# Performance work log

Hardware: AMD Instinct MI355X
Metric: run time of the kernel (lower is better)

## Reference

```python
import jax, jax.numpy as jnp
import numpy as np

NUM_HEADS = 16

def setup_inputs() -> dict:
    key = jax.random.key(0)
    ks = jax.random.split(key, 11)
    B, S, E, H, KV = 32, 4, 1024, NUM_HEADS, 4096
    d = E // H
    inp = {
        "x": jax.random.normal(ks[0], (B, S, E), dtype=jnp.float32),
        "cache_k": jax.random.normal(ks[1], (B, H, KV, d), dtype=jnp.float32),
        "cache_v": jax.random.normal(ks[2], (B, H, KV, d), dtype=jnp.float32),
        "Wq": jax.random.normal(ks[3], (E, E), dtype=jnp.float32) * (E ** -0.5),
        "bq": jax.random.normal(ks[4], (E,), dtype=jnp.float32) * 0.01,
        "Wk": jax.random.normal(ks[5], (E, E), dtype=jnp.float32) * (E ** -0.5),
        "bk": jax.random.normal(ks[6], (E,), dtype=jnp.float32) * 0.01,
        "Wv": jax.random.normal(ks[7], (E, E), dtype=jnp.float32) * (E ** -0.5),
        "bv": jax.random.normal(ks[8], (E,), dtype=jnp.float32) * 0.01,
        "Wo": jax.random.normal(ks[9], (E, E), dtype=jnp.float32) * (E ** -0.5),
        "bo": jax.random.normal(ks[10], (E,), dtype=jnp.float32) * 0.01,
    }
    return inp


def reference(x, cache_k, cache_v, Wq, bq, Wk, bk, Wv, bv, Wo, bo):
    B, S, E = x.shape
    H = NUM_HEADS
    d = E // H
    # torch Linear: y = x @ W.T + b
    def proj(W, b):
        return (x @ W.T + b).reshape(B, S, H, d).transpose(0, 2, 1, 3)  # [B,H,S,d]
    Q = proj(Wq, bq)
    K_new = proj(Wk, bk)
    V_new = proj(Wv, bv)
    K = jnp.concatenate([cache_k, K_new], axis=2)  # [B,H,KV+S,d]
    V = jnp.concatenate([cache_v, V_new], axis=2)
    scores = jnp.einsum("bhqd,bhkd->bhqk", Q, K) / jnp.sqrt(jnp.float32(d))
    attn = jax.nn.softmax(scores, axis=-1)
    out = jnp.einsum("bhqk,bhkd->bhqd", attn, V)  # [B,H,S,d]
    out = out.transpose(0, 2, 1, 3).reshape(B, S, E)
    return out @ Wo.T + bo
```

## Files before the change

### kernel.cpp

```cpp
#include <hip/hip_runtime.h>
#include <math.h>

#define B_   32
#define S_   4
#define H_   16
#define D_   64
#define E_   1024
#define KV_  4096
#define NBH  512
#define CS   512
#define NC   9
#define RECSZ 264

__global__ __launch_bounds__(256) void proj_kernel(
    const float* __restrict__ A, const float* __restrict__ W,
    const float* __restrict__ bias, float* __restrict__ out, int mode) {
    __shared__ float a_lds[4 * E_];
    __shared__ float res[256];
    const int t0 = blockIdx.x * 4;
    const int n0 = blockIdx.y * 64;
    const int tid = threadIdx.x;
    const int lane = tid & 63, wid = tid >> 6;
    const int sub = lane >> 4, cg = lane & 15, tsel = cg & 3;

    const float4* Ag = (const float4*)(A + (size_t)t0 * E_);
    float4* al = (float4*)a_lds;
    #pragma unroll
    for (int i = 0; i < 4; ++i) al[tid + 256 * i] = Ag[tid + 256 * i];
    __syncthreads();

    #pragma unroll
    for (int g = 0; g < 4; ++g) {
        const int r0 = n0 + wid * 16 + g * 4;
        const float4* wrow = (const float4*)(W + (size_t)r0 * E_);
        float ac0 = 0.f, ac1 = 0.f, ac2 = 0.f, ac3 = 0.f;
        #pragma unroll
        for (int kk = 0; kk < 16; ++kk) {
            float4 w4 = wrow[sub * 256 + kk * 16 + cg];
            float4 a0 = *(const float4*)&a_lds[0 * E_ + kk * 64 + cg * 4];
            float4 a1 = *(const float4*)&a_lds[1 * E_ + kk * 64 + cg * 4];
            float4 a2 = *(const float4*)&a_lds[2 * E_ + kk * 64 + cg * 4];
            float4 a3 = *(const float4*)&a_lds[3 * E_ + kk * 64 + cg * 4];
            ac0 += w4.x * a0.x + w4.y * a0.y + w4.z * a0.z + w4.w * a0.w;
            ac1 += w4.x * a1.x + w4.y * a1.y + w4.z * a1.z + w4.w * a1.w;
            ac2 += w4.x * a2.x + w4.y * a2.y + w4.z * a2.z + w4.w * a2.w;
            ac3 += w4.x * a3.x + w4.y * a3.y + w4.z * a3.z + w4.w * a3.w;
        }
        ac0 += __shfl_xor(ac0, 1); ac0 += __shfl_xor(ac0, 2);
        ac1 += __shfl_xor(ac1, 1); ac1 += __shfl_xor(ac1, 2);
        ac2 += __shfl_xor(ac2, 1); ac2 += __shfl_xor(ac2, 2);
        ac3 += __shfl_xor(ac3, 1); ac3 += __shfl_xor(ac3, 2);
        float v = (tsel & 1) ? ((tsel & 2) ? ac3 : ac1)
                             : ((tsel & 2) ? ac2 : ac0);
        v += __shfl_xor(v, 4); v += __shfl_xor(v, 8);
        if (cg < 4) res[cg * 64 + (wid * 16 + g * 4 + sub)] = v;
    }
    __syncthreads();

    const float val = res[tid] + bias[n0 + (tid & 63)];
    const int t = t0 + (tid >> 6), e = n0 + (tid & 63);
    if (mode == 0) {
        const int b = t >> 2, s = t & 3, h = e >> 6, dk = e & 63;
        out[((size_t)((b * H_ + h) * S_ + s)) * D_ + dk] = val;
    } else {
        out[(size_t)t * E_ + e] = val;
    }
}

__device__ __forceinline__ float wave_sum(float v) {
    #pragma unroll
    for (int off = 32; off > 0; off >>= 1) v += __shfl_xor(v, off);
    return v;
}

__global__ __launch_bounds__(256) void attn_partial_kernel(
    const float* __restrict__ Qw, const float* __restrict__ Kc,
    const float* __restrict__ Vc, const float* __restrict__ Kn,
    const float* __restrict__ Vn, float* __restrict__ part) {
    __shared__ float q_s[S_ * D_];
    __shared__ float ps[CS][4];
    __shared__ float ob[4][256];
    __shared__ float wred[4][4];
    __shared__ float msh[4], lsh[4];

    const int bh = blockIdx.x;
    const int c = blockIdx.y;
    const int tid = threadIdx.x;
    const int lane = tid & 63, wid = tid >> 6;
    const int sub = lane >> 4, cg = lane & 15, qsel = cg & 3;

    q_s[tid] = Qw[(size_t)bh * 256 + tid];
    __syncthreads();

    const float* kptr;
    const float* vptr;
    int nrows;
    if (c < 8) {
        kptr = Kc + ((size_t)bh * KV_ + c * CS) * D_;
        vptr = Vc + ((size_t)bh * KV_ + c * CS) * D_;
        nrows = CS;
    } else {
        kptr = Kn + (size_t)bh * 256;
        vptr = Vn + (size_t)bh * 256;
        nrows = S_;
    }

    const float4 q0 = *(const float4*)&q_s[0 * 64 + cg * 4];
    const float4 q1 = *(const float4*)&q_s[1 * 64 + cg * 4];
    const float4 q2 = *(const float4*)&q_s[2 * 64 + cg * 4];
    const float4 q3 = *(const float4*)&q_s[3 * 64 + cg * 4];

    float mrun = -1e30f;
    for (int r0 = wid * 4; r0 < nrows; r0 += 16) {
        float4 kv = ((const float4*)(kptr + (size_t)r0 * D_))[lane];
        float p0 = kv.x * q0.x + kv.y * q0.y + kv.z * q0.z + kv.w * q0.w;
        float p1 = kv.x * q1.x + kv.y * q1.y + kv.z * q1.z + kv.w * q1.w;
        float p2 = kv.x * q2.x + kv.y * q2.y + kv.z * q2.z + kv.w * q2.w;
        float p3 = kv.x * q3.x + kv.y * q3.y + kv.z * q3.z + kv.w * q3.w;
        p0 += __shfl_xor(p0, 1); p0 += __shfl_xor(p0, 2);
        p1 += __shfl_xor(p1, 1); p1 += __shfl_xor(p1, 2);
        p2 += __shfl_xor(p2, 1); p2 += __shfl_xor(p2, 2);
        p3 += __shfl_xor(p3, 1); p3 += __shfl_xor(p3, 2);
        float v = (qsel & 1) ? ((qsel & 2) ? p3 : p1)
                             : ((qsel & 2) ? p2 : p0);
        v += __shfl_xor(v, 4); v += __shfl_xor(v, 8);
        v *= 0.125f;
        mrun = fmaxf(mrun, v);
        if (cg < 4) ps[r0 + sub][cg] = v;
    }
    mrun = fmaxf(mrun, __shfl_xor(mrun, 16));
    mrun = fmaxf(mrun, __shfl_xor(mrun, 32));
    if (lane < 4) wred[lane][wid] = mrun;
    __syncthreads();
    if (tid < 4) {
        msh[tid] = fmaxf(fmaxf(wred[tid][0], wred[tid][1]),
                         fmaxf(wred[tid][2], wred[tid][3]));
    }
    __syncthreads();
    const float m0 = msh[0], m1 = msh[1], m2 = msh[2], m3 = msh[3];

    float4 tl = make_float4(0.f, 0.f, 0.f, 0.f);
    for (int r = tid; r < nrows; r += 256) {
        float4 s = *(float4*)ps[r];
        s.x = __expf(s.x - m0); s.y = __expf(s.y - m1);
        s.z = __expf(s.z - m2); s.w = __expf(s.w - m3);
        *(float4*)ps[r] = s;
        tl.x += s.x; tl.y += s.y; tl.z += s.z; tl.w += s.w;
    }
    tl.x = wave_sum(tl.x); tl.y = wave_sum(tl.y);
    tl.z = wave_sum(tl.z); tl.w = wave_sum(tl.w);
    if (lane == 0) {
        wred[0][wid] = tl.x; wred[1][wid] = tl.y;
        wred[2][wid] = tl.z; wred[3][wid] = tl.w;
    }
    __syncthreads();
    if (tid < 4) {
        lsh[tid] = wred[tid][0] + wred[tid][1] + wred[tid][2] + wred[tid][3];
    }
    __syncthreads();

    float4 a0 = make_float4(0.f, 0.f, 0.f, 0.f);
    float4 a1 = a0, a2 = a0, a3 = a0;
    for (int r0 = wid * 4; r0 < nrows; r0 += 16) {
        float4 vv = ((const float4*)(vptr + (size_t)r0 * D_))[lane];
        float4 p = *(const float4*)ps[r0 + sub];
        a0.x = fmaf(p.x, vv.x, a0.x); a0.y = fmaf(p.x, vv.y, a0.y);
        a0.z = fmaf(p.x, vv.z, a0.z); a0.w = fmaf(p.x, vv.w, a0.w);
        a1.x = fmaf(p.y, vv.x, a1.x); a1.y = fmaf(p.y, vv.y, a1.y);
        a1.z = fmaf(p.y, vv.z, a1.z); a1.w = fmaf(p.y, vv.w, a1.w);
        a2.x = fmaf(p.z, vv.x, a2.x); a2.y = fmaf(p.z, vv.y, a2.y);
        a2.z = fmaf(p.z, vv.z, a2.z); a2.w = fmaf(p.z, vv.w, a2.w);
        a3.x = fmaf(p.w, vv.x, a3.x); a3.y = fmaf(p.w, vv.y, a3.y);
        a3.z = fmaf(p.w, vv.z, a3.z); a3.w = fmaf(p.w, vv.w, a3.w);
    }
    a0.x += __shfl_xor(a0.x, 16); a0.x += __shfl_xor(a0.x, 32);
    a0.y += __shfl_xor(a0.y, 16); a0.y += __shfl_xor(a0.y, 32);
    a0.z += __shfl_xor(a0.z, 16); a0.z += __shfl_xor(a0.z, 32);
    a0.w += __shfl_xor(a0.w, 16); a0.w += __shfl_xor(a0.w, 32);
    a1.x += __shfl_xor(a1.x, 16); a1.x += __shfl_xor(a1.x, 32);
    a1.y += __shfl_xor(a1.y, 16); a1.y += __shfl_xor(a1.y, 32);
    a1.z += __shfl_xor(a1.z, 16); a1.z += __shfl_xor(a1.z, 32);
    a1.w += __shfl_xor(a1.w, 16); a1.w += __shfl_xor(a1.w, 32);
    a2.x += __shfl_xor(a2.x, 16); a2.x += __shfl_xor(a2.x, 32);
    a2.y += __shfl_xor(a2.y, 16); a2.y += __shfl_xor(a2.y, 32);
    a2.z += __shfl_xor(a2.z, 16); a2.z += __shfl_xor(a2.z, 32);
    a2.w += __shfl_xor(a2.w, 16); a2.w += __shfl_xor(a2.w, 32);
    a3.x += __shfl_xor(a3.x, 16); a3.x += __shfl_xor(a3.x, 32);
    a3.y += __shfl_xor(a3.y, 16); a3.y += __shfl_xor(a3.y, 32);
    a3.z += __shfl_xor(a3.z, 16); a3.z += __shfl_xor(a3.z, 32);
    a3.w += __shfl_xor(a3.w, 16); a3.w += __shfl_xor(a3.w, 32);
    if (sub == 0) {
        *(float4*)&ob[wid][0 * 64 + cg * 4] = a0;
        *(float4*)&ob[wid][1 * 64 + cg * 4] = a1;
        *(float4*)&ob[wid][2 * 64 + cg * 4] = a2;
        *(float4*)&ob[wid][3 * 64 + cg * 4] = a3;
    }
    __syncthreads();

    float* rec = part + ((size_t)bh * NC + c) * RECSZ;
    if (tid < 4) {
        rec[tid] = msh[tid];
        rec[4 + tid] = lsh[tid];
    }
    rec[8 + tid] = ob[0][tid] + ob[1][tid] + ob[2][tid] + ob[3][tid];
}

__global__ __launch_bounds__(256) void attn_combine_kernel(
    const float* __restrict__ part, float* __restrict__ attn_out) {
    const int bh = blockIdx.x;
    const int tid = threadIdx.x;
    const int q = tid >> 6, dl = tid & 63;
    const float* base = part + (size_t)bh * NC * RECSZ;

    float m = -1e30f;
    #pragma unroll
    for (int c = 0; c < NC; ++c) m = fmaxf(m, base[c * RECSZ + q]);
    float l = 0.f, o = 0.f;
    #pragma unroll
    for (int c = 0; c < NC; ++c) {
        float w = __expf(base[c * RECSZ + q] - m);
        l = fmaf(base[c * RECSZ + 4 + q], w, l);
        o = fmaf(base[c * RECSZ + 8 + tid], w, o);
    }
    const float res = o / l;
    const int b = bh >> 4, h = bh & 15;
    attn_out[((size_t)(b * S_ + q)) * E_ + h * D_ + dl] = res;
}

extern "C" void kernel_launch(void* const* d_in, const int* in_sizes, int n_in,
                              void* d_out, int out_size, void* d_ws, size_t ws_size,
                              hipStream_t stream) {
    const float* x  = (const float*)d_in[0];
    const float* ck = (const float*)d_in[1];
    const float* cv = (const float*)d_in[2];
    const float* Wq = (const float*)d_in[3];
    const float* bq = (const float*)d_in[4];
    const float* Wk = (const float*)d_in[5];
    const float* bk = (const float*)d_in[6];
    const float* Wv = (const float*)d_in[7];
    const float* bv = (const float*)d_in[8];
    const float* Wo = (const float*)d_in[9];
    const float* bo = (const float*)d_in[10];
    float* out = (float*)d_out;
    float* ws = (float*)d_ws;

    float* Qw = ws;
    float* Kn = ws + 131072;
    float* Vn = ws + 262144;
    float* part = ws + 393216;
    float* attn_out = ws + 393216 + 1216512;

    dim3 pg(32, 16), pb(256);
    hipLaunchKernelGGL(proj_kernel, pg, pb, 0, stream, x, Wq, bq, Qw, 0);
    hipLaunchKernelGGL(proj_kernel, pg, pb, 0, stream, x, Wk, bk, Kn, 0);
    hipLaunchKernelGGL(proj_kernel, pg, pb, 0, stream, x, Wv, bv, Vn, 0);
    hipLaunchKernelGGL(attn_partial_kernel, dim3(NBH, NC), dim3(256), 0, stream,
                       Qw, ck, cv, Kn, Vn, part);
    hipLaunchKernelGGL(attn_combine_kernel, dim3(NBH), dim3(256), 0, stream,
                       part, attn_out);
    hipLaunchKernelGGL(proj_kernel, pg, pb, 0, stream, attn_out, Wo, bo, out, 1);
}
```

Baseline: 244.9 us.

## Fuse split-K attention partials into single-pass online softmax with register prefetch

Replaces the three-phase partial attention (scores to LDS, block-wide max/exp/sum, then a separate P·V pass) with a single streaming loop. Each wave keeps a running max, sum and output, rescaling only when the max grows by more than a threshold. The next K and V rows are prefetched into registers to overlap loads with math. Per-wave partial results are merged once at the end, which removes the LDS score buffer and several block barriers. In exchange it adds per-iteration wave reductions and shuffles, and the lazy-rescale threshold lets exp values grow larger before rescaling.

```diff
diff --git a/kernel.cpp b/kernel.cpp
--- a/kernel.cpp
+++ b/kernel.cpp
@@ -67,9 +67,9 @@
     }
 }
 
-__device__ __forceinline__ float wave_sum(float v) {
-    #pragma unroll
-    for (int off = 32; off > 0; off >>= 1) v += __shfl_xor(v, off);
+__device__ __forceinline__ float wave_max64(float v) {
+    #pragma unroll
+    for (int off = 32; off > 0; off >>= 1) v = fmaxf(v, __shfl_xor(v, off));
     return v;
 }
 
@@ -78,10 +78,9 @@
     const float* __restrict__ Vc, const float* __restrict__ Kn,
     const float* __restrict__ Vn, float* __restrict__ part) {
     __shared__ float q_s[S_ * D_];
-    __shared__ float ps[CS][4];
     __shared__ float ob[4][256];
-    __shared__ float wred[4][4];
-    __shared__ float msh[4], lsh[4];
+    __shared__ float mw[4];
+    __shared__ float lw[4][4];
 
     const int bh = blockIdx.x;
     const int c = blockIdx.y;
@@ -110,9 +109,24 @@
     const float4 q2 = *(const float4*)&q_s[2 * 64 + cg * 4];
     const float4 q3 = *(const float4*)&q_s[3 * 64 + cg * 4];
 
-    float mrun = -1e30f;
-    for (int r0 = wid * 4; r0 < nrows; r0 += 16) {
-        float4 kv = ((const float4*)(kptr + (size_t)r0 * D_))[lane];
+    float m_run = -INFINITY;
+    float l_run = 0.f;
+    float4 a0 = make_float4(0.f, 0.f, 0.f, 0.f);
+    float4 a1 = a0, a2 = a0, a3 = a0;
+
+    int r0 = wid * 4;
+    float4 kv, vv;
+    if (r0 < nrows) {
+        kv = ((const float4*)(kptr + (size_t)r0 * D_))[lane];
+        vv = ((const float4*)(vptr + (size_t)r0 * D_))[lane];
+    }
+    while (r0 < nrows) {
+        const int r1 = r0 + 16;
+        float4 kn_ = kv, vn_ = vv;
+        if (r1 < nrows) {
+            kn_ = ((const float4*)(kptr + (size_t)r1 * D_))[lane];
+            vn_ = ((const float4*)(vptr + (size_t)r1 * D_))[lane];
+        }
         float p0 = kv.x * q0.x + kv.y * q0.y + kv.z * q0.z + kv.w * q0.w;
         float p1 = kv.x * q1.x + kv.y * q1.y + kv.z * q1.z + kv.w * q1.w;
         float p2 = kv.x * q2.x + kv.y * q2.y + kv.z * q2.z + kv.w * q2.w;
@@ -121,58 +135,43 @@
         p1 += __shfl_xor(p1, 1); p1 += __shfl_xor(p1, 2);
         p2 += __shfl_xor(p2, 1); p2 += __shfl_xor(p2, 2);
         p3 += __shfl_xor(p3, 1); p3 += __shfl_xor(p3, 2);
-        float v = (qsel & 1) ? ((qsel & 2) ? p3 : p1)
+        float s = (qsel & 1) ? ((qsel & 2) ? p3 : p1)
                              : ((qsel & 2) ? p2 : p0);
-        v += __shfl_xor(v, 4); v += __shfl_xor(v, 8);
-        v *= 0.125f;
-        mrun = fmaxf(mrun, v);
-        if (cg < 4) ps[r0 + sub][cg] = v;
-    }
-    mrun = fmaxf(mrun, __shfl_xor(mrun, 16));
-    mrun = fmaxf(mrun, __shfl_xor(mrun, 32));
-    if (lane < 4) wred[lane][wid] = mrun;
-    __syncthreads();
-    if (tid < 4) {
-        msh[tid] = fmaxf(fmaxf(wred[tid][0], wred[tid][1]),
-                         fmaxf(wred[tid][2], wred[tid][3]));
-    }
-    __syncthreads();
-    const float m0 = msh[0], m1 = msh[1], m2 = msh[2], m3 = msh[3];
-
-    float4 tl = make_float4(0.f, 0.f, 0.f, 0.f);
-    for (int r = tid; r < nrows; r += 256) {
-        float4 s = *(float4*)ps[r];
-        s.x = __expf(s.x - m0); s.y = __expf(s.y - m1);
-        s.z = __expf(s.z - m2); s.w = __expf(s.w - m3);
-        *(float4*)ps[r] = s;
-        tl.x += s.x; tl.y += s.y; tl.z += s.z; tl.w += s.w;
-    }
-    tl.x = wave_sum(tl.x); tl.y = wave_sum(tl.y);
-    tl.z = wave_sum(tl.z); tl.w = wave_sum(tl.w);
-    if (lane == 0) {
-        wred[0][wid] = tl.x; wred[1][wid] = tl.y;
-        wred[2][wid] = tl.z; wred[3][wid] = tl.w;
-    }
-    __syncthreads();
-    if (tid < 4) {
-        lsh[tid] = wred[tid][0] + wred[tid][1] + wred[tid][2] + wred[tid][3];
-    }
-    __syncthreads();
-
-    float4 a0 = make_float4(0.f, 0.f, 0.f, 0.f);
-    float4 a1 = a0, a2 = a0, a3 = a0;
-    for (int r0 = wid * 4; r0 < nrows; r0 += 16) {
-        float4 vv = ((const float4*)(vptr + (size_t)r0 * D_))[lane];
-        float4 p = *(const float4*)ps[r0 + sub];
-        a0.x = fmaf(p.x, vv.x, a0.x); a0.y = fmaf(p.x, vv.y, a0.y);
-        a0.z = fmaf(p.x, vv.z, a0.z); a0.w = fmaf(p.x, vv.w, a0.w);
-        a1.x = fmaf(p.y, vv.x, a1.x); a1.y = fmaf(p.y, vv.y, a1.y);
-        a1.z = fmaf(p.y, vv.z, a1.z); a1.w = fmaf(p.y, vv.w, a1.w);
-        a2.x = fmaf(p.z, vv.x, a2.x); a2.y = fmaf(p.z, vv.y, a2.y);
-        a2.z = fmaf(p.z, vv.z, a2.z); a2.w = fmaf(p.z, vv.w, a2.w);
-        a3.x = fmaf(p.w, vv.x, a3.x); a3.y = fmaf(p.w, vv.y, a3.y);
-        a3.z = fmaf(p.w, vv.z, a3.z); a3.w = fmaf(p.w, vv.w, a3.w);
-    }
+        s += __shfl_xor(s, 4); s += __shfl_xor(s, 8);
+        s *= 0.125f;
+
+        const float vmax = wave_max64(s);
+        if (vmax > m_run + 8.f) {
+            const float scale = __expf(m_run - vmax);
+            a0.x *= scale; a0.y *= scale; a0.z *= scale; a0.w *= scale;
+            a1.x *= scale; a1.y *= scale; a1.z *= scale; a1.w *= scale;
+            a2.x *= scale; a2.y *= scale; a2.z *= scale; a2.w *= scale;
+            a3.x *= scale; a3.y *= scale; a3.z *= scale; a3.w *= scale;
+            l_run *= scale;
+            m_run = vmax;
+        }
+        const float px = __expf(s - m_run);
+        l_run += (cg < 4) ? px : 0.f;
+
+        const int srcbase = (sub << 4);
+        const float pq0 = __shfl(px, srcbase + 0);
+        const float pq1 = __shfl(px, srcbase + 1);
+        const float pq2 = __shfl(px, srcbase + 2);
+        const float pq3 = __shfl(px, srcbase + 3);
+
+        a0.x = fmaf(pq0, vv.x, a0.x); a0.y = fmaf(pq0, vv.y, a0.y);
+        a0.z = fmaf(pq0, vv.z, a0.z); a0.w = fmaf(pq0, vv.w, a0.w);
+        a1.x = fmaf(pq1, vv.x, a1.x); a1.y = fmaf(pq1, vv.y, a1.y);
+        a1.z = fmaf(pq1, vv.z, a1.z); a1.w = fmaf(pq1, vv.w, a1.w);
+        a2.x = fmaf(pq2, vv.x, a2.x); a2.y = fmaf(pq2, vv.y, a2.y);
+        a2.z = fmaf(pq2, vv.z, a2.z); a2.w = fmaf(pq2, vv.w, a2.w);
+        a3.x = fmaf(pq3, vv.x, a3.x); a3.y = fmaf(pq3, vv.y, a3.y);
+        a3.z = fmaf(pq3, vv.z, a3.z); a3.w = fmaf(pq3, vv.w, a3.w);
+
+        kv = kn_; vv = vn_;
+        r0 = r1;
+    }
+
     a0.x += __shfl_xor(a0.x, 16); a0.x += __shfl_xor(a0.x, 32);
     a0.y += __shfl_xor(a0.y, 16); a0.y += __shfl_xor(a0.y, 32);
     a0.z += __shfl_xor(a0.z, 16); a0.z += __shfl_xor(a0.z, 32);
@@ -189,20 +188,32 @@
     a3.y += __shfl_xor(a3.y, 16); a3.y += __shfl_xor(a3.y, 32);
     a3.z += __shfl_xor(a3.z, 16); a3.z += __shfl_xor(a3.z, 32);
     a3.w += __shfl_xor(a3.w, 16); a3.w += __shfl_xor(a3.w, 32);
+
+    float l2 = l_run;
+    l2 += __shfl_xor(l2, 16); l2 += __shfl_xor(l2, 32);
+
     if (sub == 0) {
         *(float4*)&ob[wid][0 * 64 + cg * 4] = a0;
         *(float4*)&ob[wid][1 * 64 + cg * 4] = a1;
         *(float4*)&ob[wid][2 * 64 + cg * 4] = a2;
         *(float4*)&ob[wid][3 * 64 + cg * 4] = a3;
     }
-    __syncthreads();
+    if (lane < 4) lw[wid][lane] = l2;
+    if (lane == 0) mw[wid] = m_run;
+    __syncthreads();
+
+    const float M = fmaxf(fmaxf(mw[0], mw[1]), fmaxf(mw[2], mw[3]));
+    const float w0 = __expf(mw[0] - M), w1 = __expf(mw[1] - M);
+    const float w2 = __expf(mw[2] - M), w3 = __expf(mw[3] - M);
 
     float* rec = part + ((size_t)bh * NC + c) * RECSZ;
+    rec[8 + tid] = w0 * ob[0][tid] + w1 * ob[1][tid] +
+                   w2 * ob[2][tid] + w3 * ob[3][tid];
     if (tid < 4) {
-        rec[tid] = msh[tid];
-        rec[4 + tid] = lsh[tid];
-    }
-    rec[8 + tid] = ob[0][tid] + ob[1][tid] + ob[2][tid] + ob[3][tid];
+        rec[tid] = M;
+        rec[4 + tid] = w0 * lw[0][tid] + w1 * lw[1][tid] +
+                       w2 * lw[2][tid] + w3 * lw[3][tid];
+    }
 }
 
 __global__ __launch_bounds__(256) void attn_combine_kernel(
```

Result: slower. 261.0 us (+6.6%).
